# Kernel optimization log

Measured on AMD Instinct MI355X. Metric: run time of the kernel, lower is better.

The kernel has to match this reference:

```python
import jax, jax.numpy as jnp
import numpy as np
import math

B, L, DIM, H = 2, 2048, 512, 8


def setup_inputs() -> dict:
    key = jax.random.key(0)
    ks = jax.random.split(key, 8)
    s = 0.02
    return {
        "x": jax.random.normal(ks[0], (B, L, DIM), dtype=jnp.float32),
        "Wq": jax.random.normal(ks[1], (DIM, DIM), dtype=jnp.float32) * s,
        "Wk": jax.random.normal(ks[2], (DIM, DIM), dtype=jnp.float32) * s,
        "Wv": jax.random.normal(ks[3], (DIM, DIM), dtype=jnp.float32) * s,
        "Wb": jax.random.normal(ks[4], (H, DIM), dtype=jnp.float32) * s,   # content_bias weight
        "mixing": jax.random.normal(ks[5], (H, DIM), dtype=jnp.float32) * 0.2,  # UNIFORM init, std=0.2
        "Wd": jax.random.normal(ks[6], (DIM, DIM), dtype=jnp.float32) * s,
        "bd": jax.random.normal(ks[7], (DIM,), dtype=jnp.float32) * s,
    }


def reference(x, Wq, Wk, Wv, Wb, mixing, Wd, bd):
    b, l, d = x.shape
    h = mixing.shape[0]
    dh = d // h
    q = x @ Wq.T                      # [B,L,D]
    k = x @ Wk.T                      # [B,S,D]
    v = (x @ Wv.T).reshape(b, l, h, dh).transpose(0, 2, 1, 3)  # [B,H,S,dh]
    # scores[b,h,l,s] = sum_d q[b,l,d] * mixing[h,d] * k[b,s,d]
    scores = jnp.einsum("bld,hd,bsd->bhls", q, mixing, k)
    # content bias: [B,S,H] -> broadcast over query positions as [B,H,1,S]
    cb = jnp.einsum("bsd,hd->bhs", x, Wb)
    scale = math.sqrt(d / h)  # attention_head_size = dim / num_heads
    scores = (scores + cb[:, :, None, :]) / scale
    probs = jax.nn.softmax(scores, axis=-1)   # dropout disabled (eval)
    ctx = jnp.einsum("bhls,bhsd->bhld", probs, v)  # [B,H,L,dh]
    ctx = ctx.transpose(0, 2, 1, 3).reshape(b, l, d)
    return ctx @ Wd.T + bd
```

## Files before the change

kernel.cpp:

```cpp
#include <hip/hip_runtime.h>

#define B_ 2
#define L_ 2048
#define D_ 512
#define H_ 8
#define S_ 2048

typedef __attribute__((ext_vector_type(8))) short short8;
typedef __attribute__((ext_vector_type(8))) unsigned short ushort8;
typedef __attribute__((ext_vector_type(4))) unsigned short ushort4v;
typedef __attribute__((ext_vector_type(4))) float f32x4;
typedef __attribute__((ext_vector_type(16))) float f32x16;
typedef __attribute__((ext_vector_type(4))) float float4v;

__device__ __forceinline__ unsigned short f2bf(float f) {
    unsigned u = __float_as_uint(f);
    u += 0x7FFF + ((u >> 16) & 1);
    return (unsigned short)(u >> 16);
}
__device__ __forceinline__ float bf2f(unsigned short s) {
    return __uint_as_float(((unsigned)s) << 16);
}
__device__ __forceinline__ unsigned char f2fp8(float f) {
    return (unsigned char)(__builtin_amdgcn_cvt_pk_fp8_f32(f, f, 0, false) & 0xff);
}
__device__ __forceinline__ long pack8fp8(const float* v) {
    int lo = __builtin_amdgcn_cvt_pk_fp8_f32(v[0], v[1], 0, false);
    lo = __builtin_amdgcn_cvt_pk_fp8_f32(v[2], v[3], lo, true);
    int hi = __builtin_amdgcn_cvt_pk_fp8_f32(v[4], v[5], 0, false);
    hi = __builtin_amdgcn_cvt_pk_fp8_f32(v[6], v[7], hi, true);
    union { int i[2]; long l; } u;
    u.i[0] = lo; u.i[1] = hi;
    return u.l;
}
__device__ __forceinline__ int swap23(int x) {
    return (x & ~12) | ((x & 4) << 1) | ((x & 8) >> 1);
}
__device__ __forceinline__ void async16(void* lds, const void* g) {
    __builtin_amdgcn_global_load_lds(
        (const __attribute__((address_space(1))) void*)(g),
        (__attribute__((address_space(3))) void*)(lds), 16, 0, 0);
}

__global__ __launch_bounds__(256) void cvt_cb(const float* __restrict__ x,
                                              const float* __restrict__ w0, const float* __restrict__ w1,
                                              const float* __restrict__ w2, const float* __restrict__ w3,
                                              const float* __restrict__ Wb,
                                              unsigned short* __restrict__ xb,
                                              unsigned short* __restrict__ d0, unsigned short* __restrict__ d1,
                                              unsigned short* __restrict__ d2, unsigned short* __restrict__ d3,
                                              unsigned short* __restrict__ cb) {
    if (blockIdx.x < 3072) {
        int i = blockIdx.x * 256 + threadIdx.x;
        const float* s;
        unsigned short* d;
        int idx;
        if (i < 524288) { s = x; d = xb; idx = i; }
        else {
            int off = i - 524288;
            int wsel = off >> 16; idx = off & 65535;
            s = (wsel == 0) ? w0 : (wsel == 1) ? w1 : (wsel == 2) ? w2 : w3;
            d = (wsel == 0) ? d0 : (wsel == 1) ? d1 : (wsel == 2) ? d2 : d3;
        }
        float4v v = *(const float4v*)(s + (size_t)idx * 4);
        ushort4v o;
        o[0] = f2bf(v[0]); o[1] = f2bf(v[1]); o[2] = f2bf(v[2]); o[3] = f2bf(v[3]);
        *(ushort4v*)(d + (size_t)idx * 4) = o;
    } else {
        const int tid = threadIdx.x, w = tid >> 6, lane = tid & 63;
        const int row = (blockIdx.x - 3072) * 4 + w;
        const int h = lane >> 3, seg = lane & 7;
        const float* xp = x + (size_t)row * 512 + seg * 64;
        const float* wp = Wb + (size_t)h * 512 + seg * 64;
        float acc = 0.f;
        #pragma unroll
        for (int j = 0; j < 16; ++j) {
            float4v xv = *(const float4v*)(xp + j * 4);
            float4v wv = *(const float4v*)(wp + j * 4);
            acc += xv[0] * wv[0] + xv[1] * wv[1] + xv[2] * wv[2] + xv[3] * wv[3];
        }
        acc += __shfl_xor(acc, 1);
        acc += __shfl_xor(acc, 2);
        acc += __shfl_xor(acc, 4);
        if (seg == 0) {
            int b = row >> 11, s = row & 2047;
            cb[((size_t)(b * H_ + h)) * S_ + s] = f2bf(acc * 0.125f);
        }
    }
}

__device__ __forceinline__ void gemm128_core(const unsigned short* __restrict__ Ap,
                                             const unsigned short* __restrict__ Bp,
                                             short* sA, short* sB, int tid, f32x4 c[4][4]) {
    const int w = tid >> 6, lane = tid & 63, quad = lane >> 4, l15 = lane & 15;
    const int wm = (w >> 1) * 64, wn = (w & 1) * 64;
    for (int kc = 0; kc < 8; ++kc) {
        __syncthreads();
        #pragma unroll
        for (int j = 0; j < 4; ++j) {
            int i = tid + j * 256;
            int row = i >> 3, seg = i & 7;
            *(ushort8*)&sA[row * 72 + seg * 8] = *(const ushort8*)(Ap + (size_t)row * 512 + kc * 64 + seg * 8);
            *(ushort8*)&sB[row * 72 + seg * 8] = *(const ushort8*)(Bp + (size_t)row * 512 + kc * 64 + seg * 8);
        }
        __syncthreads();
        #pragma unroll
        for (int ks = 0; ks < 2; ++ks) {
            short8 a[4], b[4];
            #pragma unroll
            for (int ii = 0; ii < 4; ++ii)
                a[ii] = *(const short8*)&sA[(wm + ii * 16 + l15) * 72 + ks * 32 + quad * 8];
            #pragma unroll
            for (int jj = 0; jj < 4; ++jj)
                b[jj] = *(const short8*)&sB[(wn + jj * 16 + l15) * 72 + ks * 32 + quad * 8];
            #pragma unroll
            for (int ii = 0; ii < 4; ++ii)
                #pragma unroll
                for (int jj = 0; jj < 4; ++jj)
                    c[ii][jj] = __builtin_amdgcn_mfma_f32_16x16x32_bf16(a[ii], b[jj], c[ii][jj], 0, 0, 0);
        }
    }
}

__global__ __launch_bounds__(256) void gemm_qkv(const unsigned short* __restrict__ xb,
                                                const unsigned short* __restrict__ Wqb,
                                                const unsigned short* __restrict__ Wkb,
                                                const unsigned short* __restrict__ Wvb,
                                                unsigned short* __restrict__ qb,
                                                unsigned char* __restrict__ kpack8,
                                                unsigned short* __restrict__ vfrag) {
    __shared__ short sA[128 * 72];
    __shared__ short sB[128 * 72];
    const int m0 = blockIdx.x * 128, n0 = blockIdx.y * 128, z = blockIdx.z;
    const unsigned short* Bsel = (z == 0) ? Wqb : ((z == 1) ? Wkb : Wvb);
    f32x4 c[4][4];
    #pragma unroll
    for (int ii = 0; ii < 4; ++ii)
        #pragma unroll
        for (int jj = 0; jj < 4; ++jj) { f32x4 zv = {0.f, 0.f, 0.f, 0.f}; c[ii][jj] = zv; }
    gemm128_core(xb + (size_t)m0 * 512, Bsel + (size_t)n0 * 512, sA, sB, threadIdx.x, c);
    const int tid = threadIdx.x, w = tid >> 6, lane = tid & 63, quad = lane >> 4, l15 = lane & 15;
    const int wm = (w >> 1) * 64, wn = (w & 1) * 64;
    #pragma unroll
    for (int ii = 0; ii < 4; ++ii) {
        const int mb = m0 + wm + ii * 16 + quad * 4;
        const int bb = mb >> 11;
        if (z == 0) {
            #pragma unroll
            for (int jj = 0; jj < 4; ++jj) {
                int ncol = n0 + wn + jj * 16 + l15;
                #pragma unroll
                for (int r = 0; r < 4; ++r)
                    qb[(size_t)(mb + r) * 512 + ncol] = f2bf(c[ii][jj][r]);
            }
        } else if (z == 1) {
            #pragma unroll
            for (int jj = 0; jj < 4; ++jj) {
                int d = n0 + wn + jj * 16 + l15;
                int pair = d >> 5, fh = (d >> 4) & 1, hid = (d >> 3) & 1, jq = d & 7;
                #pragma unroll
                for (int r = 0; r < 4; ++r) {
                    int s = (mb + r) & 2047;
                    int t = s >> 5, rr = swap23(s & 31);
                    kpack8[(((size_t)(bb * 64 + t) * 16 + pair) << 10)
                           + (hid * 32 + rr) * 16 + fh * 8 + jq] = f2fp8(c[ii][jj][r] * 32.f);
                }
            }
        } else {
            const int hh = (n0 + wn) >> 6;
            const int s = mb & 2047;
            #pragma unroll
            for (int jj = 0; jj < 4; ++jj) {
                int dh = jj * 16 + l15;
                ushort4v o;
                o[0] = f2bf(c[ii][jj][0]); o[1] = f2bf(c[ii][jj][1]);
                o[2] = f2bf(c[ii][jj][2]); o[3] = f2bf(c[ii][jj][3]);
                size_t blk = ((size_t)(bb * H_ + hh) * 64 + (s >> 5)) * 4
                           + ((dh >> 5) * 2 + ((s >> 4) & 1));
                *(ushort4v*)(vfrag + blk * 512 + (dh & 31) * 8 + ((s >> 3) & 1) * 256 + (s & 7)) = o;
            }
        }
    }
}

__global__ __launch_bounds__(256) void gemm_out(const unsigned short* __restrict__ ctxb,
                                                const unsigned short* __restrict__ Wdb,
                                                const float* __restrict__ bd,
                                                float* __restrict__ out) {
    __shared__ short sA[128 * 72];
    __shared__ short sB[128 * 72];
    const int m0 = blockIdx.x * 128, n0 = blockIdx.y * 128;
    f32x4 c[4][4];
    #pragma unroll
    for (int ii = 0; ii < 4; ++ii)
        #pragma unroll
        for (int jj = 0; jj < 4; ++jj) { f32x4 zv = {0.f, 0.f, 0.f, 0.f}; c[ii][jj] = zv; }
    gemm128_core(ctxb + (size_t)m0 * 512, Wdb + (size_t)n0 * 512, sA, sB, threadIdx.x, c);
    const int tid = threadIdx.x, w = tid >> 6, lane = tid & 63, quad = lane >> 4, l15 = lane & 15;
    const int wm = (w >> 1) * 64, wn = (w & 1) * 64;
    #pragma unroll
    for (int ii = 0; ii < 4; ++ii) {
        const int mb = m0 + wm + ii * 16 + quad * 4;
        #pragma unroll
        for (int jj = 0; jj < 4; ++jj) {
            int ncol = n0 + wn + jj * 16 + l15;
            float bias = bd[ncol];
            #pragma unroll
            for (int r = 0; r < 4; ++r)
                out[(size_t)(mb + r) * 512 + ncol] = c[ii][jj][r] + bias;
        }
    }
}

__global__ __launch_bounds__(256, 2) void flash_attn(const unsigned short* __restrict__ qb,
                                                     const unsigned char* __restrict__ kpack8,
                                                     const unsigned short* __restrict__ vfrag,
                                                     const unsigned short* __restrict__ cb_all,
                                                     const float* __restrict__ mixing,
                                                     _Float16* __restrict__ Opart,
                                                     float* __restrict__ lpart) {
    __shared__ char sK[4][8192];
    const int bid = blockIdx.x;
    const int half = bid & 1, b = (bid >> 1) & 1, h = (bid >> 2) & 7, qt = bid >> 5;
    const int tid = threadIdx.x, w = tid >> 6, lane = tid & 63;
    const int l31 = lane & 31, hi = lane >> 5;
    const int q0 = qt * 128 + w * 32;
    const unsigned char* kbase = kpack8 + (((size_t)(b * 64 + half * 32)) << 14);
    const unsigned short* vfb = vfrag + ((size_t)(b * H_ + h) * 64 + half * 32) * 2048;
    const unsigned short* cbq = cb_all + (size_t)(b * H_ + h) * S_ + half * 1024;
    const float* mixh = mixing + h * D_;

    long qq[32];
    {
        const unsigned short* qrow = qb + ((size_t)(b * L_) + q0 + l31) * D_ + hi * 8;
        #pragma unroll
        for (int i = 0; i < 32; ++i) {
            ushort8 qv = *(const ushort8*)(qrow + i * 16);
            float4v ma = *(const float4v*)(mixh + i * 16 + hi * 8);
            float4v mb = *(const float4v*)(mixh + i * 16 + hi * 8 + 4);
            float v[8];
            v[0] = bf2f(qv[0]) * ma[0] * 16.f;
            v[1] = bf2f(qv[1]) * ma[1] * 16.f;
            v[2] = bf2f(qv[2]) * ma[2] * 16.f;
            v[3] = bf2f(qv[3]) * ma[3] * 16.f;
            v[4] = bf2f(qv[4]) * mb[0] * 16.f;
            v[5] = bf2f(qv[5]) * mb[1] * 16.f;
            v[6] = bf2f(qv[6]) * mb[2] * 16.f;
            v[7] = bf2f(qv[7]) * mb[3] * 16.f;
            qq[i] = pack8fp8(v);
        }
    }
    asm volatile("s_waitcnt vmcnt(0)" ::: "memory");

    f32x16 acco0, acco1;
    #pragma unroll
    for (int i = 0; i < 16; ++i) { acco0[i] = 0.f; acco1[i] = 0.f; }
    float lsum = 0.f;
    f32x16 accsA, accsB;
    short8 av00, av01, av10, av11;
    ushort8 cbr0, cbr1, cbr2, cbr3;

    auto stageK = [&](int p) {
        const char* src = (const char*)kpack8 + (((size_t)(b * 64 + half * 32)) << 14) + (size_t)p * 8192;
        char* dst = &sK[p & 3][0];
        #pragma unroll
        for (int ii = 0; ii < 2; ++ii)
            async16(dst + w * 1024 + ii * 4096, src + w * 1024 + ii * 4096 + (size_t)lane * 16);
    };
    auto ldV = [&](int t) {
        const unsigned short* vp = vfb + (size_t)t * 2048 + lane * 8;
        av00 = *(const short8*)(vp);
        av01 = *(const short8*)(vp + 512);
        av10 = *(const short8*)(vp + 1024);
        av11 = *(const short8*)(vp + 1536);
        asm volatile("" ::: "memory");
    };
    auto ldCB = [&](int t) {
        const unsigned short* cp = cbq + t * 32;
        cbr0 = *(const ushort8*)(cp);
        cbr1 = *(const ushort8*)(cp + 8);
        cbr2 = *(const ushort8*)(cp + 16);
        cbr3 = *(const ushort8*)(cp + 24);
        asm volatile("" ::: "memory");
    };
    auto qk_chunk = [&](const char* buf, int qbase) {
        __builtin_amdgcn_s_setprio(1);
        #pragma unroll
        for (int p = 0; p < 8; ++p) {
            long a0, a1;
            {
                const long* ap = (const long*)&buf[p * 1024 + lane * 16];
                a0 = ap[0];
                a1 = ap[1];
            }
            accsA = __builtin_amdgcn_mfma_f32_32x32x16_fp8_fp8(a0, qq[qbase + 2 * p], accsA, 0, 0, 0);
            accsB = __builtin_amdgcn_mfma_f32_32x32x16_fp8_fp8(a1, qq[qbase + 2 * p + 1], accsB, 0, 0, 0);
        }
        __builtin_amdgcn_s_setprio(0);
    };
    auto softmax_pv = [&]() {
        float p[16];
        #pragma unroll
        for (int R = 0; R < 16; ++R) {
            const int cr = (R & 3) + 8 * (R >> 2);
            const int il = cr - 4 * ((R >> 2) & 1);
            const int ih = il + 8;
            unsigned short ca = (il < 8)  ? cbr0[il & 7] : cbr2[il & 7];
            unsigned short cbb = (ih < 16) ? cbr1[ih & 7] : cbr3[ih & 7];
            float cbv = bf2f(hi ? cbb : ca);
            float pe = __expf((accsA[R] + accsB[R]) * (1.0f / 4096.0f) + cbv);
            p[R] = pe;
            lsum += pe;
        }
        union { unsigned int u[4]; short8 s8; } P0, P1;
        #pragma unroll
        for (int j = 0; j < 4; ++j) {
            P0.u[j] = __builtin_amdgcn_perm(__float_as_uint(p[2 * j + 1]) + 0x8000u,
                                            __float_as_uint(p[2 * j]) + 0x8000u, 0x07060302u);
            P1.u[j] = __builtin_amdgcn_perm(__float_as_uint(p[8 + 2 * j + 1]) + 0x8000u,
                                            __float_as_uint(p[8 + 2 * j]) + 0x8000u, 0x07060302u);
        }
        __builtin_amdgcn_s_setprio(1);
        acco0 = __builtin_amdgcn_mfma_f32_32x32x16_bf16(av00, P0.s8, acco0, 0, 0, 0);
        acco0 = __builtin_amdgcn_mfma_f32_32x32x16_bf16(av01, P1.s8, acco0, 0, 0, 0);
        acco1 = __builtin_amdgcn_mfma_f32_32x32x16_bf16(av10, P0.s8, acco1, 0, 0, 0);
        acco1 = __builtin_amdgcn_mfma_f32_32x32x16_bf16(av11, P1.s8, acco1, 0, 0, 0);
        __builtin_amdgcn_s_setprio(0);
    };

    stageK(0); stageK(1); stageK(2);

    for (int t = 0; t < 31; ++t) {
        #pragma unroll
        for (int i = 0; i < 16; ++i) { accsA[i] = 0.f; accsB[i] = 0.f; }
        const char* be = &sK[(t & 1) << 1][0];
        const char* bo = &sK[((t & 1) << 1) | 1][0];
        asm volatile("s_waitcnt vmcnt(4)" ::: "memory");
        __builtin_amdgcn_s_barrier();
        ldV(t);
        ldCB(t);
        stageK(2 * t + 3);
        qk_chunk(be, 0);
        asm volatile("s_waitcnt vmcnt(12)" ::: "memory");
        __builtin_amdgcn_s_barrier();
        if (t < 30) stageK(2 * t + 4);
        qk_chunk(bo, 16);
        softmax_pv();
    }
    {
        #pragma unroll
        for (int i = 0; i < 16; ++i) { accsA[i] = 0.f; accsB[i] = 0.f; }
        asm volatile("s_waitcnt vmcnt(4)" ::: "memory");
        __builtin_amdgcn_s_barrier();
        ldV(31);
        ldCB(31);
        qk_chunk(&sK[2][0], 0);
        asm volatile("s_waitcnt vmcnt(8)" ::: "memory");
        __builtin_amdgcn_s_barrier();
        qk_chunk(&sK[3][0], 16);
        softmax_pv();
    }

    lsum += __shfl_xor(lsum, 32);
    if (hi == 0) lpart[(size_t)bid * 128 + w * 32 + l31] = lsum;
    #pragma unroll
    for (int R = 0; R < 16; ++R) {
        int dh = (R & 3) + 8 * (R >> 2) + 4 * hi;
        Opart[((size_t)bid * 64 + dh) * 128 + w * 32 + l31] = (_Float16)acco0[R];
        Opart[((size_t)bid * 64 + 32 + dh) * 128 + w * 32 + l31] = (_Float16)acco1[R];
    }
}

__global__ __launch_bounds__(256) void merge_ctx(const _Float16* __restrict__ Opart,
                                                 const float* __restrict__ lpart,
                                                 unsigned short* __restrict__ ctxb) {
    int t = blockIdx.x * 256 + threadIdx.x;
    int qq = t & 127, dh4 = (t >> 7) & 15, qt = (t >> 11) & 15, h = (t >> 15) & 7, b = t >> 18;
    int base = (qt << 5) | (h << 2) | (b << 1);
    float l = lpart[(size_t)base * 128 + qq] + lpart[(size_t)(base + 1) * 128 + qq];
    float inv = 1.f / l;
    ushort4v o;
    #pragma unroll
    for (int e = 0; e < 4; ++e) {
        int dh = dh4 * 4 + e;
        float v = (float)Opart[((size_t)base * 64 + dh) * 128 + qq]
                + (float)Opart[((size_t)(base + 1) * 64 + dh) * 128 + qq];
        o[e] = f2bf(v * inv);
    }
    *(ushort4v*)(ctxb + ((size_t)(b * L_) + qt * 128 + qq) * 512 + h * 64 + dh4 * 4) = o;
}

extern "C" void kernel_launch(void* const* d_in, const int* in_sizes, int n_in,
                              void* d_out, int out_size, void* d_ws, size_t ws_size,
                              hipStream_t stream) {
    (void)in_sizes; (void)n_in; (void)out_size; (void)ws_size;
    const float* x      = (const float*)d_in[0];
    const float* Wq     = (const float*)d_in[1];
    const float* Wk     = (const float*)d_in[2];
    const float* Wv     = (const float*)d_in[3];
    const float* Wb     = (const float*)d_in[4];
    const float* mixing = (const float*)d_in[5];
    const float* Wd     = (const float*)d_in[6];
    const float* bd     = (const float*)d_in[7];
    float* out = (float*)d_out;

    char* ws = (char*)d_ws;
    const size_t MiB = 1048576;
    unsigned short* xb     = (unsigned short*)(ws);
    unsigned short* qb     = (unsigned short*)(ws + 4 * MiB);
    unsigned char*  kpack8 = (unsigned char*)(ws + 8 * MiB);
    unsigned short* vfrag  = (unsigned short*)(ws + 10 * MiB);
    unsigned short* ctxb   = (unsigned short*)(ws + 14 * MiB);
    unsigned short* Wqb    = (unsigned short*)(ws + 18 * MiB);
    unsigned short* Wkb    = (unsigned short*)(ws + 18 * MiB + 512 * 1024);
    unsigned short* Wvb    = (unsigned short*)(ws + 19 * MiB);
    unsigned short* Wdb    = (unsigned short*)(ws + 19 * MiB + 512 * 1024);
    unsigned short* cbuf   = (unsigned short*)(ws + 20 * MiB);
    float* lpart           = (float*)(ws + 20 * MiB + 256 * 1024);
    _Float16* Opart        = (_Float16*)(ws + 21 * MiB);

    cvt_cb<<<4096, 256, 0, stream>>>(x, Wq, Wk, Wv, Wd, Wb, xb, Wqb, Wkb, Wvb, Wdb, cbuf);
    gemm_qkv<<<dim3(32, 4, 3), 256, 0, stream>>>(xb, Wqb, Wkb, Wvb, qb, kpack8, vfrag);
    flash_attn<<<512, 256, 0, stream>>>(qb, kpack8, vfrag, cbuf, mixing, Opart, lpart);
    merge_ctx<<<2048, 256, 0, stream>>>(Opart, lpart, ctxb);
    gemm_out<<<dim3(32, 4), 256, 0, stream>>>(ctxb, Wdb, bd, out);
}
```

Measured before the change: 200.6 us.

## Software-pipeline QK and softmax-PV across tiles with double-buffered score accumulators

Splits the score accumulators into two ping-pong sets so the softmax and PV MFMAs of tile t-1 run interleaved with the QK MFMAs of tile t, instead of strictly after them. The loop is unrolled by two with macros, the prologue and epilogue are restructured, and the vmcnt waits are retuned for the new order of V, content-bias and K loads. This aims to hide the exp/convert latency behind matrix work. In exchange it costs 32 more accumulator registers at a 2-waves-per-SIMD launch bound, and the hand-counted vmcnt values must stay correct.

```diff
diff --git a/kernel.cpp b/kernel.cpp
--- a/kernel.cpp
+++ b/kernel.cpp
@@ -225,7 +225,6 @@
     const int tid = threadIdx.x, w = tid >> 6, lane = tid & 63;
     const int l31 = lane & 31, hi = lane >> 5;
     const int q0 = qt * 128 + w * 32;
-    const unsigned char* kbase = kpack8 + (((size_t)(b * 64 + half * 32)) << 14);
     const unsigned short* vfb = vfrag + ((size_t)(b * H_ + h) * 64 + half * 32) * 2048;
     const unsigned short* cbq = cb_all + (size_t)(b * H_ + h) * S_ + half * 1024;
     const float* mixh = mixing + h * D_;
@@ -256,7 +255,7 @@
     #pragma unroll
     for (int i = 0; i < 16; ++i) { acco0[i] = 0.f; acco1[i] = 0.f; }
     float lsum = 0.f;
-    f32x16 accsA, accsB;
+    f32x16 aA0, aB0, aA1, aB1;
     short8 av00, av01, av10, av11;
     ushort8 cbr0, cbr1, cbr2, cbr3;
 
@@ -283,7 +282,7 @@
         cbr3 = *(const ushort8*)(cp + 24);
         asm volatile("" ::: "memory");
     };
-    auto qk_chunk = [&](const char* buf, int qbase) {
+    auto qk_chunk = [&](const char* buf, int qbase, f32x16& A, f32x16& B) {
         __builtin_amdgcn_s_setprio(1);
         #pragma unroll
         for (int p = 0; p < 8; ++p) {
@@ -293,12 +292,12 @@
                 a0 = ap[0];
                 a1 = ap[1];
             }
-            accsA = __builtin_amdgcn_mfma_f32_32x32x16_fp8_fp8(a0, qq[qbase + 2 * p], accsA, 0, 0, 0);
-            accsB = __builtin_amdgcn_mfma_f32_32x32x16_fp8_fp8(a1, qq[qbase + 2 * p + 1], accsB, 0, 0, 0);
+            A = __builtin_amdgcn_mfma_f32_32x32x16_fp8_fp8(a0, qq[qbase + 2 * p], A, 0, 0, 0);
+            B = __builtin_amdgcn_mfma_f32_32x32x16_fp8_fp8(a1, qq[qbase + 2 * p + 1], B, 0, 0, 0);
         }
         __builtin_amdgcn_s_setprio(0);
     };
-    auto softmax_pv = [&]() {
+    auto softmax_pv = [&](const f32x16& A, const f32x16& B) {
         float p[16];
         #pragma unroll
         for (int R = 0; R < 16; ++R) {
@@ -308,7 +307,7 @@
             unsigned short ca = (il < 8)  ? cbr0[il & 7] : cbr2[il & 7];
             unsigned short cbb = (ih < 16) ? cbr1[ih & 7] : cbr3[ih & 7];
             float cbv = bf2f(hi ? cbb : ca);
-            float pe = __expf((accsA[R] + accsB[R]) * (1.0f / 4096.0f) + cbv);
+            float pe = __expf((A[R] + B[R]) * (1.0f / 4096.0f) + cbv);
             p[R] = pe;
             lsum += pe;
         }
@@ -327,38 +326,60 @@
         acco1 = __builtin_amdgcn_mfma_f32_32x32x16_bf16(av11, P1.s8, acco1, 0, 0, 0);
         __builtin_amdgcn_s_setprio(0);
     };
+    auto zero16 = [](f32x16& v) {
+        #pragma unroll
+        for (int i = 0; i < 16; ++i) v[i] = 0.f;
+    };
 
     stageK(0); stageK(1); stageK(2);
 
-    for (int t = 0; t < 31; ++t) {
-        #pragma unroll
-        for (int i = 0; i < 16; ++i) { accsA[i] = 0.f; accsB[i] = 0.f; }
-        const char* be = &sK[(t & 1) << 1][0];
-        const char* bo = &sK[((t & 1) << 1) | 1][0];
-        asm volatile("s_waitcnt vmcnt(4)" ::: "memory");
+    zero16(aA0); zero16(aB0);
+    asm volatile("s_waitcnt vmcnt(4)" ::: "memory");
+    __builtin_amdgcn_s_barrier();
+    stageK(3);
+    qk_chunk(&sK[0][0], 0, aA0, aB0);
+    ldV(0); ldCB(0);
+    asm volatile("s_waitcnt vmcnt(12)" ::: "memory");
+    __builtin_amdgcn_s_barrier();
+    stageK(4);
+    qk_chunk(&sK[1][0], 16, aA0, aB0);
+
+    #define E_TILE(T, CA, CB, PA, PB)                                            \
+        zero16(CA); zero16(CB);                                                  \
+        asm volatile("s_waitcnt vmcnt(12)" ::: "memory");       \
+        __builtin_amdgcn_s_barrier();                                            \
+        stageK(2 * (T) + 3);                                                     \
+        qk_chunk(&sK[((T) & 1) << 1][0], 0, CA, CB);                             \
+        asm volatile("s_waitcnt vmcnt(4)" ::: "memory");    \
+        softmax_pv(PA, PB);                                                      \
+        ldV(T); ldCB(T);
+    #define O_TILE(T, CA, CB)                                                    \
+        __builtin_amdgcn_s_barrier();                                            \
+        if ((T) < 30) stageK(2 * (T) + 4);                                       \
+        qk_chunk(&sK[(((T) & 1) << 1) | 1][0], 16, CA, CB);
+
+    for (int tt = 1; tt < 30; tt += 2) {
+        E_TILE(tt, aA1, aB1, aA0, aB0);
+        O_TILE(tt, aA1, aB1);
+        E_TILE(tt + 1, aA0, aB0, aA1, aB1);
+        O_TILE(tt + 1, aA0, aB0);
+    }
+    #undef E_TILE
+    #undef O_TILE
+
+    {
+        zero16(aA1); zero16(aB1);
+        asm volatile("s_waitcnt vmcnt(10)" ::: "memory");
         __builtin_amdgcn_s_barrier();
-        ldV(t);
-        ldCB(t);
-        stageK(2 * t + 3);
-        qk_chunk(be, 0);
-        asm volatile("s_waitcnt vmcnt(12)" ::: "memory");
-        __builtin_amdgcn_s_barrier();
-        if (t < 30) stageK(2 * t + 4);
-        qk_chunk(bo, 16);
-        softmax_pv();
-    }
-    {
-        #pragma unroll
-        for (int i = 0; i < 16; ++i) { accsA[i] = 0.f; accsB[i] = 0.f; }
-        asm volatile("s_waitcnt vmcnt(4)" ::: "memory");
-        __builtin_amdgcn_s_barrier();
-        ldV(31);
-        ldCB(31);
-        qk_chunk(&sK[2][0], 0);
+        qk_chunk(&sK[2][0], 0, aA1, aB1);
+        asm volatile("s_waitcnt vmcnt(2)" ::: "memory");
+        softmax_pv(aA0, aB0);
+        ldV(31); ldCB(31);
         asm volatile("s_waitcnt vmcnt(8)" ::: "memory");
         __builtin_amdgcn_s_barrier();
-        qk_chunk(&sK[3][0], 16);
-        softmax_pv();
+        qk_chunk(&sK[3][0], 16, aA1, aB1);
+        asm volatile("s_waitcnt vmcnt(0)" ::: "memory");
+        softmax_pv(aA1, aB1);
     }
 
     lsum += __shfl_xor(lsum, 32);
```

Result: no change. 200.0 us (-0.3%).
